# Kernel optimization log

Measured on AMD Instinct MI355X. Metric: run time of the kernel, lower is better.

Reference implementation:

```python
import jax, jax.numpy as jnp
import numpy as np

EPS = 1e-5
DIM = 128
SCALE = DIM ** (-0.5)


def setup_inputs() -> dict:
    key = jax.random.key(0)
    k1, k2, k3 = jax.random.split(key, 3)
    B, N, D = 2, 128 * 128, DIM
    Q = N // 4
    x = jax.random.normal(k1, (B, N, D), dtype=jnp.float32)
    gamma = jnp.ones((D,), dtype=jnp.float32)
    beta = jnp.zeros((D,), dtype=jnp.float32)
    queries = jax.random.normal(k2, (Q, D), dtype=jnp.float32)
    W = jax.random.normal(k3, (2 * D, D), dtype=jnp.float32) * (1.0 / np.sqrt(D))
    return {"x": x, "gamma": gamma, "beta": beta, "queries": queries, "W": W}


def reference(x, gamma, beta, queries, W):
    # LayerNorm over last dim (eps matches torch default 1e-5)
    mu = jnp.mean(x, axis=-1, keepdims=True)
    var = jnp.mean(jnp.square(x - mu), axis=-1, keepdims=True)
    xn = (x - mu) * jax.lax.rsqrt(var + EPS) * gamma + beta  # [B, N, D]
    # learned-query cross attention: sim = Q @ xn^T * scale -> softmax -> @ xn
    sim = jnp.einsum('qd,bnd->bqn', queries, xn) * SCALE     # [B, Q, N]
    attn = jax.nn.softmax(sim, axis=-1)
    out = jnp.einsum('bqn,bnd->bqd', attn, xn)               # [B, Q, D]
    # trailing linear: dim -> 2*dim, no bias
    return jnp.einsum('bqd,ed->bqe', out, W)                 # [B, Q, 2D]
```

## Files before the change

### kernel.cpp

```cpp
#include <hip/hip_runtime.h>
#include <stdint.h>

#define Nn 16384
#define Dd 128
#define Qq 4096
#define Ee 256
#define NSPLIT 8
#define NCHUNK 2048
#define KV 64
#define NITER 32

typedef __bf16 bf16x8 __attribute__((ext_vector_type(8)));
typedef float floatx16 __attribute__((ext_vector_type(16)));

__device__ __forceinline__ float fexp2(float x) {
#if __has_builtin(__builtin_amdgcn_exp2f)
  return __builtin_amdgcn_exp2f(x);
#else
  return exp2f(x);
#endif
}
__device__ __forceinline__ unsigned pk_bf(float lo, float hi) {
  return __builtin_amdgcn_perm(__float_as_uint(hi) + 0x8000u,
                               __float_as_uint(lo) + 0x8000u, 0x07060302u);
}
__device__ __forceinline__ void stage16(const void* g, void* lds_uniform) {
  __builtin_amdgcn_global_load_lds(
      (const __attribute__((address_space(1))) unsigned int*)g,
      (__attribute__((address_space(3))) unsigned int*)lds_uniform, 16, 0, 0);
}

__global__ __launch_bounds__(256) void k_lnt(
    const float* __restrict__ x, const float* __restrict__ gamma,
    const float* __restrict__ beta, const float* __restrict__ queries,
    const float* __restrict__ W, unsigned* __restrict__ xn,
    unsigned short* __restrict__ xnT, unsigned short* __restrict__ qb,
    unsigned short* __restrict__ wb) {
  __shared__ __align__(16) uint2 lds2[64 * 32];
  const int tid = threadIdx.x;
  const int bid = blockIdx.x;
  const int b = bid >> 8, n0 = (bid & 255) * 64;
  const int r = tid >> 2, qd = tid & 3;

  const float4* xp = (const float4*)(x + ((size_t)(b * Nn + n0 + r)) * Dd + qd * 32);
  float4 v[8];
  float s = 0.f, s2 = 0.f;
#pragma unroll
  for (int i = 0; i < 8; ++i) {
    v[i] = xp[i];
    s += (v[i].x + v[i].y) + (v[i].z + v[i].w);
    s2 += (v[i].x * v[i].x + v[i].y * v[i].y) + (v[i].z * v[i].z + v[i].w * v[i].w);
  }
  s += __shfl_xor(s, 1); s2 += __shfl_xor(s2, 1);
  s += __shfl_xor(s, 2); s2 += __shfl_xor(s2, 2);
  float mu = s * (1.0f / 128.0f);
  float var = s2 * (1.0f / 128.0f) - mu * mu;
  float rs = rsqrtf(var + 1e-5f);

  const float4* gp = (const float4*)(gamma + qd * 32);
  const float4* bp = (const float4*)(beta + qd * 32);
  unsigned pk[16];
#pragma unroll
  for (int i = 0; i < 8; ++i) {
    float4 g = gp[i], bt = bp[i];
    pk[2 * i] = pk_bf((v[i].x - mu) * rs * g.x + bt.x, (v[i].y - mu) * rs * g.y + bt.y);
    pk[2 * i + 1] = pk_bf((v[i].z - mu) * rs * g.z + bt.z, (v[i].w - mu) * rs * g.w + bt.w);
  }
  unsigned* xrow = xn + ((size_t)(b * Nn + n0 + r)) * 64;
#pragma unroll
  for (int j = 0; j < 4; ++j)
    *(uint4*)(xrow + (((qd * 4 + j) ^ (r & 7)) * 4)) =
        make_uint4(pk[4 * j], pk[4 * j + 1], pk[4 * j + 2], pk[4 * j + 3]);
  const int rk = r & 31;
#pragma unroll
  for (int kk = 0; kk < 8; ++kk)
    lds2[r * 32 + ((qd * 8 + kk) ^ rk)] = make_uint2(pk[2 * kk], pk[2 * kk + 1]);
  __syncthreads();
  const int dq = tid >> 3, nc = tid & 7;
  uint2 U[8];
#pragma unroll
  for (int j = 0; j < 8; ++j) {
    int rr = nc * 8 + j;
    U[j] = lds2[rr * 32 + (dq ^ (rr & 31))];
  }
#pragma unroll
  for (int e = 0; e < 4; ++e) {
    int d = dq * 4 + e;
    unsigned a0 = (e & 2) ? U[0].y : U[0].x, a1 = (e & 2) ? U[1].y : U[1].x;
    unsigned a2 = (e & 2) ? U[2].y : U[2].x, a3 = (e & 2) ? U[3].y : U[3].x;
    unsigned a4 = (e & 2) ? U[4].y : U[4].x, a5 = (e & 2) ? U[5].y : U[5].x;
    unsigned a6 = (e & 2) ? U[6].y : U[6].x, a7 = (e & 2) ? U[7].y : U[7].x;
    unsigned sel = (e & 1) ? 0x07060302u : 0x05040100u;
    uint4 o;
    o.x = __builtin_amdgcn_perm(a1, a0, sel);
    o.y = __builtin_amdgcn_perm(a3, a2, sel);
    o.z = __builtin_amdgcn_perm(a5, a4, sel);
    o.w = __builtin_amdgcn_perm(a7, a6, sel);
    *(uint4*)(xnT + ((size_t)(b * Dd + d)) * Nn + n0 + (nc ^ (d & 7)) * 8) = o;
  }
  const float QSC = 0.08838834764831845f * 1.4426950408889634f;
  const int total4 = (Qq * Dd + Ee * Dd) / 4;
  for (int u = bid * 256 + tid; u < total4; u += 512 * 256) {
    if (u < Qq * Dd / 4) {
      float4 v4 = ((const float4*)queries)[u];
      ((uint2*)qb)[u] = make_uint2(pk_bf(v4.x * QSC, v4.y * QSC),
                                   pk_bf(v4.z * QSC, v4.w * QSC));
    } else {
      float4 v4 = ((const float4*)W)[u - Qq * Dd / 4];
      ((uint2*)wb)[u - Qq * Dd / 4] =
          make_uint2(pk_bf(v4.x, v4.y), pk_bf(v4.z, v4.w));
    }
  }
}

__global__ __launch_bounds__(256, 2) void k_attn(
    const unsigned short* __restrict__ xn,
    const unsigned short* __restrict__ xnT,
    const unsigned short* __restrict__ qb,
    float* __restrict__ o_part,
    float* __restrict__ l_part) {
  __shared__ __align__(16) char lds[49152];
  char* lds_x = lds;
  char* lds_xt = lds + 16384;
  char* lds_p = lds + 32768;

  const int bid = blockIdx.x;
  const int split = bid & 7, qt = (bid >> 3) & 31, b = bid >> 8;
  const int tid = threadIdx.x;
  const int wave = tid >> 6, lane = tid & 63;
  const int col = lane & 31, half = lane >> 5;
  const int ck = col & 7;
  const int qwbase = qt * 128 + wave * 32;

  bf16x8 qf[8];
#pragma unroll
  for (int s = 0; s < 8; ++s)
    qf[s] = *(const bf16x8*)(qb + (size_t)(qwbase + col) * Dd + s * 16 + half * 8);

  const floatx16 fz = {0.f,0.f,0.f,0.f,0.f,0.f,0.f,0.f,0.f,0.f,0.f,0.f,0.f,0.f,0.f,0.f};
  floatx16 O[4];
#pragma unroll
  for (int d = 0; d < 4; ++d) O[d] = fz;
  float lsum = 0.f;

  const char* gx = (const char*)xn + (size_t)b * Nn * 256;
  const char* gxt = (const char*)xnT + (size_t)b * Dd * Nn * 2;
  char* ldsp_w = lds_p + wave * 4096;

  for (int i = 0; i < NITER; ++i) {
    const int nb = split * NCHUNK + i * KV;
    const char* xsrc = gx + (size_t)nb * 256;
#pragma unroll
    for (int p = 0; p < 4; ++p) {
      int m = wave * 4 + p;
      stage16(xsrc + m * 1024 + lane * 16, lds_x + m * 1024);
    }
#pragma unroll
    for (int p = 0; p < 4; ++p) {
      int m = wave * 4 + p;
      const char* g = gxt + (size_t)(m * 8 + (lane >> 3)) * (Nn * 2) +
                      (size_t)nb * 2 + (lane & 7) * 16;
      stage16(g, lds_xt + m * 1024);
    }
    __syncthreads();

    floatx16 S[2];
    S[0] = fz; S[1] = fz;
#pragma unroll
    for (int s = 0; s < 8; ++s)
#pragma unroll
      for (int mt = 0; mt < 2; ++mt) {
        bf16x8 ax = *(const bf16x8*)(lds_x + (32 * mt + col) * 256 +
                                     (((2 * s + half) ^ ck) * 16));
        S[mt] = __builtin_amdgcn_mfma_f32_32x32x16_bf16(ax, qf[s], S[mt], 0, 0, 0);
      }

#pragma unroll
    for (int mt = 0; mt < 2; ++mt)
#pragma unroll
      for (int t = 0; t < 4; ++t) {
        float p0 = fexp2(S[mt][4 * t]);
        float p1 = fexp2(S[mt][4 * t + 1]);
        float p2 = fexp2(S[mt][4 * t + 2]);
        float p3 = fexp2(S[mt][4 * t + 3]);
        lsum += (p0 + p1) + (p2 + p3);
        int w = 4 * mt + t;
        *(uint2*)(ldsp_w + col * 128 + ((w ^ ck) * 16) + half * 8) =
            make_uint2(pk_bf(p0, p1), pk_bf(p2, p3));
      }

#pragma unroll
    for (int s2 = 0; s2 < 4; ++s2) {
      bf16x8 ap = *(const bf16x8*)(ldsp_w + col * 128 + (((2 * s2 + half) ^ ck) * 16));
#pragma unroll
      for (int dn = 0; dn < 4; ++dn) {
        bf16x8 bx = *(const bf16x8*)(lds_xt + (32 * dn + col) * 128 +
                                     (((2 * s2 + half) ^ ck) * 16));
        O[dn] = __builtin_amdgcn_mfma_f32_32x32x16_bf16(ap, bx, O[dn], 0, 0, 0);
      }
    }
    __syncthreads();
  }

  float lt = lsum + __shfl_xor(lsum, 32);
  if (half == 0)
    l_part[(size_t)(b * NSPLIT + split) * Qq + qwbase + col] = lt;
  float* op = o_part + ((size_t)(b * NSPLIT + split) * Qq + qwbase) * Dd;
#pragma unroll
  for (int dn = 0; dn < 4; ++dn)
#pragma unroll
    for (int r = 0; r < 16; ++r) {
      int q = (r & 3) + 8 * (r >> 2) + 4 * half;
      op[(size_t)q * Dd + dn * 32 + col] = O[dn][r];
    }
}

__global__ __launch_bounds__(256) void k_comb(
    const float* __restrict__ o_part, const float* __restrict__ l_part,
    const unsigned short* __restrict__ wb, float* __restrict__ out) {
  __shared__ __align__(16) char lds_a[32 * 256];
  __shared__ float lds_linv[32];
  const int bid = blockIdx.x;
  const int b = bid >> 7, qc = bid & 127;
  const int qbase = qc * 32;
  const int tid = threadIdx.x;
  const int wave = tid >> 6, lane = tid & 63;
  const int col = lane & 31, half = lane >> 5;
  const int ck = col & 7;

  if (tid < 32) {
    float l = 0.f;
#pragma unroll
    for (int s = 0; s < 8; ++s)
      l += l_part[(size_t)(b * 8 + s) * Qq + qbase + tid];
    lds_linv[tid] = 1.0f / l;
  }
  __syncthreads();

#pragma unroll
  for (int i = 0; i < 4; ++i) {
    int idx = i * 256 + tid;
    int q = idx >> 5, d4 = idx & 31;
    float4 acc = make_float4(0.f, 0.f, 0.f, 0.f);
#pragma unroll
    for (int s = 0; s < 8; ++s) {
      float4 v = *(const float4*)(o_part + ((size_t)(b * 8 + s) * Qq + qbase + q) * Dd + d4 * 4);
      acc.x += v.x; acc.y += v.y; acc.z += v.z; acc.w += v.w;
    }
    float li = lds_linv[q];
    int w = d4 >> 1;
    int pos = (w & 8) | ((w ^ (q & 7)) & 7);
    *(uint2*)(lds_a + q * 256 + pos * 16 + (d4 & 1) * 8) =
        make_uint2(pk_bf(acc.x * li, acc.y * li), pk_bf(acc.z * li, acc.w * li));
  }
  __syncthreads();

  bf16x8 af[8];
#pragma unroll
  for (int s = 0; s < 8; ++s) {
    int u = 2 * s + half;
    int pos = (u & 8) | ((u ^ ck) & 7);
    af[s] = *(const bf16x8*)(lds_a + col * 256 + pos * 16);
  }

  const floatx16 fz = {0.f,0.f,0.f,0.f,0.f,0.f,0.f,0.f,0.f,0.f,0.f,0.f,0.f,0.f,0.f,0.f};
#pragma unroll
  for (int et = 0; et < 2; ++et) {
    floatx16 C = fz;
    int e_row = wave * 64 + et * 32 + col;
#pragma unroll
    for (int s = 0; s < 8; ++s) {
      bf16x8 bw = *(const bf16x8*)(wb + (size_t)e_row * Dd + s * 16 + half * 8);
      C = __builtin_amdgcn_mfma_f32_32x32x16_bf16(af[s], bw, C, 0, 0, 0);
    }
#pragma unroll
    for (int r = 0; r < 16; ++r) {
      int q = qbase + (r & 3) + 8 * (r >> 2) + 4 * half;
      out[((size_t)b * Qq + q) * Ee + wave * 64 + et * 32 + col] = C[r];
    }
  }
}

extern "C" void kernel_launch(void* const* d_in, const int* in_sizes, int n_in,
                              void* d_out, int out_size, void* d_ws, size_t ws_size,
                              hipStream_t stream) {
  const float* x = (const float*)d_in[0];
  const float* gamma = (const float*)d_in[1];
  const float* beta = (const float*)d_in[2];
  const float* queries = (const float*)d_in[3];
  const float* W = (const float*)d_in[4];
  float* out = (float*)d_out;

  char* w = (char*)d_ws;
  unsigned short* xn = (unsigned short*)(w);
  unsigned short* xnT = (unsigned short*)(w + 8388608);
  unsigned short* qb = (unsigned short*)(w + 16777216);
  unsigned short* wb = (unsigned short*)(w + 17825792);
  float* o_part = (float*)(w + 17891328);
  float* l_part = (float*)(w + 51445760);

  k_lnt<<<dim3(512), dim3(256), 0, stream>>>(x, gamma, beta, queries, W,
                                             (unsigned*)xn, xnT, qb, wb);
  k_attn<<<dim3(512), dim3(256), 0, stream>>>(xn, xnT, qb, o_part, l_part);
  k_comb<<<dim3(256), dim3(256), 0, stream>>>(o_part, l_part, wb, out);
}
```

Before: 167.7 us.

## Double-buffer attention K/V staging and pass P via permlane swaps

The attention loop now double-buffers the x and x-transposed tiles in LDS, issuing the async global-to-LDS loads for the next chunk before computing on the current one. This is meant to hide global load latency behind the MFMA work, and it drops one barrier per iteration. The probability tile P is no longer written to and read back from LDS: the bf16-packed registers are exchanged between wave halves with permlane32_swap, falling back to shuffles when that builtin is unavailable. s_setprio hints are also added around the MFMA sections. LDS use grows from 48 KB to 64 KB per block, which may limit occupancy under launch_bounds(256,2).

```diff
diff --git a/kernel.cpp b/kernel.cpp
--- a/kernel.cpp
+++ b/kernel.cpp
@@ -12,6 +12,7 @@
 
 typedef __bf16 bf16x8 __attribute__((ext_vector_type(8)));
 typedef float floatx16 __attribute__((ext_vector_type(16)));
+typedef unsigned uintx2 __attribute__((ext_vector_type(2)));
 
 __device__ __forceinline__ float fexp2(float x) {
 #if __has_builtin(__builtin_amdgcn_exp2f)
@@ -28,6 +29,20 @@
   __builtin_amdgcn_global_load_lds(
       (const __attribute__((address_space(1))) unsigned int*)g,
       (__attribute__((address_space(3))) unsigned int*)lds_uniform, 16, 0, 0);
+}
+__device__ __forceinline__ void plswap(unsigned a, unsigned b, int hi,
+                                       unsigned& r0, unsigned& r1) {
+#if __has_builtin(__builtin_amdgcn_permlane32_swap)
+  uintx2 r = __builtin_amdgcn_permlane32_swap(a, b, false, false);
+  r0 = r[0];
+  r1 = r[1];
+  (void)hi;
+#else
+  unsigned ax = __shfl_xor(a, 32);
+  unsigned bx = __shfl_xor(b, 32);
+  r0 = hi ? bx : a;
+  r1 = hi ? b : ax;
+#endif
 }
 
 __global__ __launch_bounds__(256) void k_lnt(
@@ -119,10 +134,7 @@
     const unsigned short* __restrict__ qb,
     float* __restrict__ o_part,
     float* __restrict__ l_part) {
-  __shared__ __align__(16) char lds[49152];
-  char* lds_x = lds;
-  char* lds_xt = lds + 16384;
-  char* lds_p = lds + 32768;
+  __shared__ __align__(16) char lds[2][32768];
 
   const int bid = blockIdx.x;
   const int split = bid & 7, qt = (bid >> 3) & 31, b = bid >> 8;
@@ -145,36 +157,63 @@
 
   const char* gx = (const char*)xn + (size_t)b * Nn * 256;
   const char* gxt = (const char*)xnT + (size_t)b * Dd * Nn * 2;
-  char* ldsp_w = lds_p + wave * 4096;
-
-  for (int i = 0; i < NITER; ++i) {
-    const int nb = split * NCHUNK + i * KV;
+
+  {
+    const int nb = split * NCHUNK;
     const char* xsrc = gx + (size_t)nb * 256;
 #pragma unroll
     for (int p = 0; p < 4; ++p) {
       int m = wave * 4 + p;
-      stage16(xsrc + m * 1024 + lane * 16, lds_x + m * 1024);
+      stage16(xsrc + m * 1024 + lane * 16, &lds[0][0] + m * 1024);
     }
 #pragma unroll
     for (int p = 0; p < 4; ++p) {
       int m = wave * 4 + p;
       const char* g = gxt + (size_t)(m * 8 + (lane >> 3)) * (Nn * 2) +
                       (size_t)nb * 2 + (lane & 7) * 16;
-      stage16(g, lds_xt + m * 1024);
-    }
-    __syncthreads();
+      stage16(g, &lds[0][0] + 16384 + m * 1024);
+    }
+  }
+  asm volatile("s_waitcnt vmcnt(0)" ::: "memory");
+  __builtin_amdgcn_s_barrier();
+
+  int cur = 0;
+#pragma unroll 1
+  for (int i = 0; i < NITER; ++i) {
+    if (i + 1 < NITER) {
+      char* bufn = &lds[0][0] + ((cur ^ 1) << 15);
+      const int nb = split * NCHUNK + (i + 1) * KV;
+      const char* xsrc = gx + (size_t)nb * 256;
+#pragma unroll
+      for (int p = 0; p < 4; ++p) {
+        int m = wave * 4 + p;
+        stage16(xsrc + m * 1024 + lane * 16, bufn + m * 1024);
+      }
+#pragma unroll
+      for (int p = 0; p < 4; ++p) {
+        int m = wave * 4 + p;
+        const char* g = gxt + (size_t)(m * 8 + (lane >> 3)) * (Nn * 2) +
+                        (size_t)nb * 2 + (lane & 7) * 16;
+        stage16(g, bufn + 16384 + m * 1024);
+      }
+    }
+    const char* lx = &lds[0][0] + (cur << 15);
+    const char* lxt = lx + 16384;
 
     floatx16 S[2];
     S[0] = fz; S[1] = fz;
+    __builtin_amdgcn_s_setprio(1);
 #pragma unroll
     for (int s = 0; s < 8; ++s)
 #pragma unroll
       for (int mt = 0; mt < 2; ++mt) {
-        bf16x8 ax = *(const bf16x8*)(lds_x + (32 * mt + col) * 256 +
+        bf16x8 ax = *(const bf16x8*)(lx + (32 * mt + col) * 256 +
                                      (((2 * s + half) ^ ck) * 16));
         S[mt] = __builtin_amdgcn_mfma_f32_32x32x16_bf16(ax, qf[s], S[mt], 0, 0, 0);
       }
-
+    __builtin_amdgcn_s_setprio(0);
+
+    unsigned P[2][4][2];
 #pragma unroll
     for (int mt = 0; mt < 2; ++mt)
 #pragma unroll
@@ -184,22 +223,33 @@
         float p2 = fexp2(S[mt][4 * t + 2]);
         float p3 = fexp2(S[mt][4 * t + 3]);
         lsum += (p0 + p1) + (p2 + p3);
-        int w = 4 * mt + t;
-        *(uint2*)(ldsp_w + col * 128 + ((w ^ ck) * 16) + half * 8) =
-            make_uint2(pk_bf(p0, p1), pk_bf(p2, p3));
-      }
-
+        P[mt][t][0] = pk_bf(p0, p1);
+        P[mt][t][1] = pk_bf(p2, p3);
+      }
+
+    __builtin_amdgcn_s_setprio(1);
 #pragma unroll
     for (int s2 = 0; s2 < 4; ++s2) {
-      bf16x8 ap = *(const bf16x8*)(ldsp_w + col * 128 + (((2 * s2 + half) ^ ck) * 16));
+      const int mt = s2 >> 1, ge = 2 * (s2 & 1), go = ge + 1;
+      unsigned w0, w1, w2, w3;
+      plswap(P[mt][ge][0], P[mt][go][0], half, w0, w2);
+      plswap(P[mt][ge][1], P[mt][go][1], half, w1, w3);
+      union { uint4 u; bf16x8 v; } ap;
+      ap.u = make_uint4(w0, w1, w2, w3);
 #pragma unroll
       for (int dn = 0; dn < 4; ++dn) {
-        bf16x8 bx = *(const bf16x8*)(lds_xt + (32 * dn + col) * 128 +
+        bf16x8 bx = *(const bf16x8*)(lxt + (32 * dn + col) * 128 +
                                      (((2 * s2 + half) ^ ck) * 16));
-        O[dn] = __builtin_amdgcn_mfma_f32_32x32x16_bf16(ap, bx, O[dn], 0, 0, 0);
-      }
-    }
-    __syncthreads();
+        O[dn] = __builtin_amdgcn_mfma_f32_32x32x16_bf16(ap.v, bx, O[dn], 0, 0, 0);
+      }
+    }
+    __builtin_amdgcn_s_setprio(0);
+
+    if (i + 1 < NITER) {
+      asm volatile("s_waitcnt vmcnt(0)" ::: "memory");
+      __builtin_amdgcn_s_barrier();
+    }
+    cur ^= 1;
   }
 
   float lt = lsum + __shfl_xor(lsum, 32);
```

New measurement: 160.5 us. -4.3%, faster.
